# Kernel tuning notes

Measured on AMD Instinct MI355X. Metric: run time of the kernel, lower is better.

Reference implementation:

```python
import jax, jax.numpy as jnp
import numpy as np

jax.config.update("jax_enable_x64", True)  # hash arithmetic needs 64-bit ints

P = 56598313          # RzLinear.P (prime for the hash)
INPUT_DIM = 4096
OUTPUT_DIM = 4096
COMPRESS_RATIO = 0.0625
HASH_SIZE = int(INPUT_DIM * OUTPUT_DIM * COMPRESS_RATIO)  # 1,048,576
N_TOKENS = 8192


def setup_inputs() -> dict:
    key = jax.random.key(0)
    kx, kw, kr = jax.random.split(key, 3)
    x = jax.random.normal(kx, (N_TOKENS, INPUT_DIM), dtype=jnp.float32)
    hashed_weight = jax.random.normal(kw, (HASH_SIZE,), dtype=jnp.float32) * 0.02
    # _generate_random_numbers: [P, r1, r2, r3] with r_i forced even via r + r % 2
    r = jax.random.randint(kr, (3,), 0, P, dtype=jnp.int64)
    r = r + r % 2
    random_numbers = jnp.concatenate([jnp.array([P], dtype=jnp.int64), r])
    bias = jnp.zeros((OUTPUT_DIM,), dtype=jnp.float32)
    return {"x": x, "hashed_weight": hashed_weight,
            "random_numbers": random_numbers, "bias": bias}


def _hash_indices(random_numbers):
    # ROBE-Z hash (chunk_size=1): idx[k, n] = ((k*r3 + n*r2 + r1) % P) % HASH_SIZE
    r0 = random_numbers[0]
    r1 = random_numbers[1]
    r2 = random_numbers[2]
    r3 = random_numbers[3]
    k = jnp.arange(INPUT_DIM, dtype=jnp.int64)[:, None]   # (K, 1)
    n = jnp.arange(OUTPUT_DIM, dtype=jnp.int64)[None, :]  # (1, N)
    return ((k * r3 + n * r2 + r1) % r0) % HASH_SIZE       # (K, N)


def reference(x, hashed_weight, random_numbers, bias):
    idx = _hash_indices(random_numbers)
    W = hashed_weight[idx]          # gather-reconstructed (input_dim, output_dim)
    return x @ W + bias             # (N_TOKENS, output_dim)
```

## Files before the change

### kernel.cpp

```cpp
#include <hip/hip_runtime.h>
#include <stdint.h>


#define P_CONST 56598313u
#define HASH_MASK 0xFFFFFu
#define M_DIM 8192
#define N_DIM 4096
#define K_DIM 4096
#define BK 32
#define KSTEPS (K_DIM / BK)

typedef __attribute__((ext_vector_type(8))) short bf16x8;
typedef __attribute__((ext_vector_type(4))) float f32x4;
typedef __attribute__((ext_vector_type(4))) unsigned int u32x4;

__device__ __forceinline__ unsigned short f2bf(float f) {
    unsigned int u = __float_as_uint(f);
    return (unsigned short)((u + 0x7FFFu + ((u >> 16) & 1u)) >> 16);
}

struct RN { unsigned long long r1, r2, r3; };

__device__ __forceinline__ RN decode_rn(const void* rn_raw) {
    RN o;
    const long long* rn64 = (const long long*)rn_raw;
    if (rn64[0] == 56598313LL) {
        o.r1 = (unsigned long long)rn64[1];
        o.r2 = (unsigned long long)rn64[2];
        o.r3 = (unsigned long long)rn64[3];
    } else {
        const int* rn32 = (const int*)rn_raw;
        o.r1 = (unsigned long long)(unsigned int)rn32[1];
        o.r2 = (unsigned long long)(unsigned int)rn32[2];
        o.r3 = (unsigned long long)(unsigned int)rn32[3];
    }
    return o;
}

__device__ __forceinline__ void load16(const void* g, void* l) {
    __builtin_amdgcn_global_load_lds(
        (const __attribute__((address_space(1))) void*)g,
        (__attribute__((address_space(3))) void*)l,
        16, 0, 0);
}

__global__ __launch_bounds__(256) void prep(const float* __restrict__ x,
                                            const float* __restrict__ table,
                                            const void* __restrict__ rn_raw,
                                            unsigned short* __restrict__ Wt,
                                            unsigned short* __restrict__ Xb) {
    const int b = blockIdx.x;
    const int t = threadIdx.x;
    if (b % 5 == 0) {
        RN rn = decode_rn(rn_raw);
        const unsigned int stepu = (unsigned int)(rn.r3 % P_CONST);
        const unsigned int n = (unsigned int)(b / 5);
        const unsigned long long base =
            ((unsigned long long)n * rn.r2 + rn.r1) % P_CONST;
        const int k0 = t * 8;
        unsigned int c0 =
            (unsigned int)((base + (unsigned long long)k0 * stepu) % P_CONST);
        unsigned int c1 =
            (unsigned int)((base + (unsigned long long)(k0 + 2048) * stepu) % P_CONST);
        float f[16];
#pragma unroll
        for (int i = 0; i < 8; ++i) {
            f[i] = table[c0 & HASH_MASK];
            c0 += stepu; if (c0 >= P_CONST) c0 -= P_CONST;
            f[8 + i] = table[c1 & HASH_MASK];
            c1 += stepu; if (c1 >= P_CONST) c1 -= P_CONST;
        }
        union { unsigned short s[8]; u32x4 v; } o0, o1;
#pragma unroll
        for (int i = 0; i < 8; ++i) { o0.s[i] = f2bf(f[i]); o1.s[i] = f2bf(f[8 + i]); }
        unsigned short* dst = Wt + (size_t)n * K_DIM + k0;
        __builtin_nontemporal_store(o0.v, (u32x4*)dst);
        __builtin_nontemporal_store(o1.v, (u32x4*)(dst + 2048));
    } else {
        const int cb = b - b / 5 - 1;
        const size_t i8 = ((size_t)cb * 256 + t) * 8;
        const f32x4 a = __builtin_nontemporal_load((const f32x4*)(x + i8));
        const f32x4 c = __builtin_nontemporal_load((const f32x4*)(x + i8 + 4));
        union { unsigned short s[8]; u32x4 v; } o;
        o.s[0] = f2bf(a.x); o.s[1] = f2bf(a.y); o.s[2] = f2bf(a.z); o.s[3] = f2bf(a.w);
        o.s[4] = f2bf(c.x); o.s[5] = f2bf(c.y); o.s[6] = f2bf(c.z); o.s[7] = f2bf(c.w);
        __builtin_nontemporal_store(o.v, (u32x4*)(Xb + i8));
    }
}

__global__ __launch_bounds__(512, 2) void gemm_bt8(
    const unsigned short* __restrict__ A,
    const unsigned short* __restrict__ Bt,
    const float* __restrict__ bias,
    float* __restrict__ C) {
    __shared__ __align__(16) unsigned short lA[4][256 * BK];
    __shared__ __align__(16) unsigned short lB[4][256 * BK];

    const int t = threadIdx.x;
    const int bid0 = blockIdx.x;
    const int sb = (bid0 & 7) * 64 + (bid0 >> 3);
    const int m0 = (sb >> 4) * 256;
    const int n0 = (sb & 15) * 256;

    const int lane = t & 63;
    const int wid = t >> 6;
    const int wr = wid >> 2;
    const int wc = wid & 3;
    const int lm = lane & 15;
    const int q = lane >> 4;
    const int qswz = (q ^ ((lm >> 1) & 3)) << 4;

    const int p0 = t * 16;
    const int p1 = p0 + 8192;
    const int l0 = p0 ^ ((p0 >> 3) & 0x30);
    const int l1 = p1 ^ ((p1 >> 3) & 0x30);
    const int r0 = l0 >> 6, c0 = (l0 & 63) >> 1;
    const int r1 = l1 >> 6, c1 = (l1 & 63) >> 1;

    const unsigned short* Abase = A + (size_t)m0 * K_DIM;
    const unsigned short* Bbase = Bt + (size_t)n0 * K_DIM;

    f32x4 acc[8][4] = {};

#define STAGE_A(KS) do { const int b__ = (KS) & 3;                              \
    load16(Abase + (size_t)r0 * K_DIM + (KS) * BK + c0, (char*)&lA[b__][0] + p0);\
    load16(Abase + (size_t)r1 * K_DIM + (KS) * BK + c1, (char*)&lA[b__][0] + p1);\
} while (0)
#define STAGE_B(KS) do { const int b__ = (KS) & 3;                              \
    load16(Bbase + (size_t)r0 * K_DIM + (KS) * BK + c0, (char*)&lB[b__][0] + p0);\
    load16(Bbase + (size_t)r1 * K_DIM + (KS) * BK + c1, (char*)&lB[b__][0] + p1);\
} while (0)

#define STEP_BODY(KS, STG) do {                                                 \
    __builtin_amdgcn_s_barrier();                                               \
    asm volatile("" ::: "memory");                                              \
    const char* bufA = (const char*)&lA[(KS) & 3][0];                           \
    const char* bufB = (const char*)&lB[(KS) & 3][0];                           \
    bf16x8 af[8], bfr[4];                                                       \
    _Pragma("unroll")                                                           \
    for (int i = 0; i < 8; ++i)                                                 \
        af[i] = *(const bf16x8*)(bufA + (((wr * 128 + i * 16 + lm) << 6) | qswz));\
    _Pragma("unroll")                                                           \
    for (int j = 0; j < 4; ++j)                                                 \
        bfr[j] = *(const bf16x8*)(bufB + (((wc * 64 + j * 16 + lm) << 6) | qswz));\
    if (STG) { STAGE_A((KS) + 3); STAGE_B((KS) + 3); }                          \
    asm volatile("s_waitcnt lgkmcnt(0)" ::: "memory");                          \
    __builtin_amdgcn_sched_barrier(0);                                          \
    __builtin_amdgcn_s_setprio(1);                                              \
    _Pragma("unroll")                                                           \
    for (int i = 0; i < 8; ++i)                                                 \
        _Pragma("unroll")                                                       \
        for (int j = 0; j < 4; ++j)                                             \
            acc[i][j] = __builtin_amdgcn_mfma_f32_16x16x32_bf16(                \
                af[i], bfr[j], acc[i][j], 0, 0, 0);                             \
    __builtin_amdgcn_s_setprio(0);                                              \
} while (0)

    STAGE_A(0); STAGE_B(0);
    STAGE_A(1); STAGE_B(1);
    STAGE_A(2); STAGE_B(2);

#pragma unroll 1
    for (int ks = 0; ks < KSTEPS - 2; ++ks) {
        asm volatile("s_waitcnt vmcnt(8)" ::: "memory");
        STEP_BODY(ks, (ks < KSTEPS - 3));
    }
    asm volatile("s_waitcnt vmcnt(4)" ::: "memory");
    STEP_BODY(KSTEPS - 2, false);
    asm volatile("s_waitcnt vmcnt(0)" ::: "memory");
    STEP_BODY(KSTEPS - 1, false);

#undef STEP_BODY
#undef STAGE_A
#undef STAGE_B

#pragma unroll
    for (int j = 0; j < 4; ++j) {
        const int col = n0 + wc * 64 + j * 16 + lm;
        const float bv = bias[col];
#pragma unroll
        for (int i = 0; i < 8; ++i) {
            const int row = m0 + wr * 128 + i * 16 + q * 4;
#pragma unroll
            for (int r = 0; r < 4; ++r)
                __builtin_nontemporal_store(
                    acc[i][j][r] + bv, &C[(size_t)(row + r) * N_DIM + col]);
        }
    }
}

__global__ __launch_bounds__(256) void gemm_fused(const float* __restrict__ X,
                                                  const float* __restrict__ table,
                                                  const void* __restrict__ rn_raw,
                                                  const float* __restrict__ bias,
                                                  float* __restrict__ C) {
    RN rn = decode_rn(rn_raw);
    const unsigned int stepu = (unsigned int)(rn.r3 % P_CONST);
    const unsigned int step32 =
        (unsigned int)(((unsigned long long)stepu * 32ull) % P_CONST);

    __shared__ __align__(16) unsigned short lA[128 * 32];
    __shared__ __align__(16) unsigned short lB[128 * 32];
    const int t = threadIdx.x;
    const int m0 = blockIdx.y * 128;
    const int n0 = blockIdx.x * 128;
    const int lane = t & 63;
    const int w = t >> 6;
    const int wr = w >> 1, wc = w & 1;
    const int lm = lane & 15, q = lane >> 4;

    unsigned int curB[2];
    int rowB[2], colB[2];
#pragma unroll
    for (int e = 0; e < 2; ++e) {
        const int c = t + e * 256;
        rowB[e] = c >> 2;
        colB[e] = (c & 3) * 8;
        const unsigned long long base =
            ((unsigned long long)(n0 + rowB[e]) * rn.r2 + rn.r1) % P_CONST;
        curB[e] =
            (unsigned int)((base + (unsigned long long)colB[e] * stepu) % P_CONST);
    }

    f32x4 acc[4][4] = {};

    for (int k0 = 0; k0 < K_DIM; k0 += 32) {
#pragma unroll
        for (int c = t; c < 1024; c += 256) {
            const int row = c >> 3, col = (c & 7) * 4;
            const float4 v =
                *(const float4*)(X + (size_t)(m0 + row) * K_DIM + k0 + col);
            ushort4 o;
            o.x = f2bf(v.x); o.y = f2bf(v.y); o.z = f2bf(v.z); o.w = f2bf(v.w);
            *(ushort4*)&lA[row * 32 + col] = o;
        }
#pragma unroll
        for (int e = 0; e < 2; ++e) {
            unsigned int cur = curB[e];
            union { unsigned short s[8]; uint4 v; } o;
#pragma unroll
            for (int i = 0; i < 8; ++i) {
                o.s[i] = f2bf(table[cur & HASH_MASK]);
                cur += stepu;
                if (cur >= P_CONST) cur -= P_CONST;
            }
            curB[e] += step32;
            if (curB[e] >= P_CONST) curB[e] -= P_CONST;
            *(uint4*)&lB[rowB[e] * 32 + colB[e]] = o.v;
        }
        __syncthreads();

        bf16x8 af[4], bfr[4];
#pragma unroll
        for (int i = 0; i < 4; ++i)
            af[i] = *(const bf16x8*)&lA[(wr * 64 + i * 16 + lm) * 32 + q * 8];
#pragma unroll
        for (int j = 0; j < 4; ++j)
            bfr[j] = *(const bf16x8*)&lB[(wc * 64 + j * 16 + lm) * 32 + q * 8];
#pragma unroll
        for (int i = 0; i < 4; ++i)
#pragma unroll
            for (int j = 0; j < 4; ++j)
                acc[i][j] = __builtin_amdgcn_mfma_f32_16x16x32_bf16(
                    af[i], bfr[j], acc[i][j], 0, 0, 0);
        __syncthreads();
    }

#pragma unroll
    for (int j = 0; j < 4; ++j) {
        const int col = n0 + wc * 64 + j * 16 + lm;
        const float bv = bias[col];
#pragma unroll
        for (int i = 0; i < 4; ++i) {
            const int row = m0 + wr * 64 + i * 16 + q * 4;
#pragma unroll
            for (int r = 0; r < 4; ++r)
                C[(size_t)(row + r) * N_DIM + col] = acc[i][j][r] + bv;
        }
    }
}

extern "C" void kernel_launch(void* const* d_in, const int* in_sizes, int n_in,
                              void* d_out, int out_size, void* d_ws, size_t ws_size,
                              hipStream_t stream) {
    const float* x = (const float*)d_in[0];
    const float* hw = (const float*)d_in[1];
    const void* rn = d_in[2];
    const float* bias = (const float*)d_in[3];
    float* out = (float*)d_out;

    const size_t wt_bytes = (size_t)N_DIM * K_DIM * 2;
    const size_t xb_bytes = (size_t)M_DIM * K_DIM * 2;

    if (ws_size >= wt_bytes + xb_bytes) {
        unsigned short* Wt = (unsigned short*)d_ws;
        unsigned short* Xb = (unsigned short*)((char*)d_ws + wt_bytes);
        prep<<<20480, 256, 0, stream>>>(x, hw, rn, Wt, Xb);
        gemm_bt8<<<dim3((M_DIM / 256) * (N_DIM / 256)), 512, 0, stream>>>(Xb, Wt, bias, out);
    } else {
        gemm_fused<<<dim3(N_DIM / 128, M_DIM / 128), 256, 0, stream>>>(x, hw, rn, bias, out);
    }
}
```

Baseline: 556.3 us.

## Restructure GEMM pipeline to 64-wide K tiles and merge prep block roles

The GEMM main loop moves from a 4-deep ring of 32-wide K slices to double-buffered 64-wide K tiles, each split into two halves. Compute is interleaved in quarter-tile MFMA groups with more barriers, and the next tile is issued in two stages. The prep kernel stops splitting blocks between weight gathering and x conversion; every block now does both, gathering 4 weight entries and converting 8 x values per thread. The aim is fewer loop iterations and balanced prep work, at the cost of a shallower prefetch distance and extra barriers per tile.

New measurement: 636.7 us. 1.14x slower.

```diff
diff --git a/kernel.cpp b/kernel.cpp
--- a/kernel.cpp
+++ b/kernel.cpp
@@ -7,12 +7,12 @@
 #define M_DIM 8192
 #define N_DIM 4096
 #define K_DIM 4096
-#define BK 32
-#define KSTEPS (K_DIM / BK)
+#define KT (K_DIM / 64)
 
 typedef __attribute__((ext_vector_type(8))) short bf16x8;
 typedef __attribute__((ext_vector_type(4))) float f32x4;
 typedef __attribute__((ext_vector_type(4))) unsigned int u32x4;
+typedef __attribute__((ext_vector_type(2))) unsigned int u32x2;
 
 __device__ __forceinline__ unsigned short f2bf(float f) {
     unsigned int u = __float_as_uint(f);
@@ -51,50 +51,40 @@
                                             unsigned short* __restrict__ Xb) {
     const int b = blockIdx.x;
     const int t = threadIdx.x;
-    if (b % 5 == 0) {
-        RN rn = decode_rn(rn_raw);
-        const unsigned int stepu = (unsigned int)(rn.r3 % P_CONST);
-        const unsigned int n = (unsigned int)(b / 5);
-        const unsigned long long base =
-            ((unsigned long long)n * rn.r2 + rn.r1) % P_CONST;
-        const int k0 = t * 8;
-        unsigned int c0 =
-            (unsigned int)((base + (unsigned long long)k0 * stepu) % P_CONST);
-        unsigned int c1 =
-            (unsigned int)((base + (unsigned long long)(k0 + 2048) * stepu) % P_CONST);
-        float f[16];
-#pragma unroll
-        for (int i = 0; i < 8; ++i) {
-            f[i] = table[c0 & HASH_MASK];
-            c0 += stepu; if (c0 >= P_CONST) c0 -= P_CONST;
-            f[8 + i] = table[c1 & HASH_MASK];
-            c1 += stepu; if (c1 >= P_CONST) c1 -= P_CONST;
-        }
-        union { unsigned short s[8]; u32x4 v; } o0, o1;
-#pragma unroll
-        for (int i = 0; i < 8; ++i) { o0.s[i] = f2bf(f[i]); o1.s[i] = f2bf(f[8 + i]); }
-        unsigned short* dst = Wt + (size_t)n * K_DIM + k0;
-        __builtin_nontemporal_store(o0.v, (u32x4*)dst);
-        __builtin_nontemporal_store(o1.v, (u32x4*)(dst + 2048));
-    } else {
-        const int cb = b - b / 5 - 1;
-        const size_t i8 = ((size_t)cb * 256 + t) * 8;
-        const f32x4 a = __builtin_nontemporal_load((const f32x4*)(x + i8));
-        const f32x4 c = __builtin_nontemporal_load((const f32x4*)(x + i8 + 4));
-        union { unsigned short s[8]; u32x4 v; } o;
-        o.s[0] = f2bf(a.x); o.s[1] = f2bf(a.y); o.s[2] = f2bf(a.z); o.s[3] = f2bf(a.w);
-        o.s[4] = f2bf(c.x); o.s[5] = f2bf(c.y); o.s[6] = f2bf(c.z); o.s[7] = f2bf(c.w);
-        __builtin_nontemporal_store(o.v, (u32x4*)(Xb + i8));
-    }
-}
-
-__global__ __launch_bounds__(512, 2) void gemm_bt8(
+    RN rn = decode_rn(rn_raw);
+    const unsigned int stepu = (unsigned int)(rn.r3 % P_CONST);
+    const unsigned int n = (unsigned int)(b >> 2);
+    const int kb = ((b & 3) << 10) + (t << 2);
+    const unsigned long long base =
+        ((unsigned long long)n * rn.r2 + rn.r1) % P_CONST;
+    unsigned int cur =
+        (unsigned int)((base + (unsigned long long)kb * stepu) % P_CONST);
+    const float g0 = table[cur & HASH_MASK];
+    cur += stepu; if (cur >= P_CONST) cur -= P_CONST;
+    const float g1 = table[cur & HASH_MASK];
+    cur += stepu; if (cur >= P_CONST) cur -= P_CONST;
+    const float g2 = table[cur & HASH_MASK];
+    cur += stepu; if (cur >= P_CONST) cur -= P_CONST;
+    const float g3 = table[cur & HASH_MASK];
+    const size_t i8 = ((size_t)b * 256 + t) * 8;
+    const f32x4 a = __builtin_nontemporal_load((const f32x4*)(x + i8));
+    const f32x4 c = __builtin_nontemporal_load((const f32x4*)(x + i8 + 4));
+    union { unsigned short s[8]; u32x4 v; } o;
+    o.s[0] = f2bf(a.x); o.s[1] = f2bf(a.y); o.s[2] = f2bf(a.z); o.s[3] = f2bf(a.w);
+    o.s[4] = f2bf(c.x); o.s[5] = f2bf(c.y); o.s[6] = f2bf(c.z); o.s[7] = f2bf(c.w);
+    __builtin_nontemporal_store(o.v, (u32x4*)(Xb + i8));
+    union { unsigned short s[4]; u32x2 v; } w;
+    w.s[0] = f2bf(g0); w.s[1] = f2bf(g1); w.s[2] = f2bf(g2); w.s[3] = f2bf(g3);
+    __builtin_nontemporal_store(w.v, (u32x2*)(Wt + (size_t)n * K_DIM + kb));
+}
+
+__global__ __launch_bounds__(512, 2) void gemm_bt64(
     const unsigned short* __restrict__ A,
     const unsigned short* __restrict__ Bt,
     const float* __restrict__ bias,
     float* __restrict__ C) {
-    __shared__ __align__(16) unsigned short lA[4][256 * BK];
-    __shared__ __align__(16) unsigned short lB[4][256 * BK];
+    __shared__ __align__(16) unsigned short lA[2][2][256 * 32];
+    __shared__ __align__(16) unsigned short lB[2][2][256 * 32];
 
     const int t = threadIdx.x;
     const int bid0 = blockIdx.x;
@@ -122,57 +112,96 @@
 
     f32x4 acc[8][4] = {};
 
-#define STAGE_A(KS) do { const int b__ = (KS) & 3;                              \
-    load16(Abase + (size_t)r0 * K_DIM + (KS) * BK + c0, (char*)&lA[b__][0] + p0);\
-    load16(Abase + (size_t)r1 * K_DIM + (KS) * BK + c1, (char*)&lA[b__][0] + p1);\
+#define STAGE(T, KH) do {                                                       \
+    const int db__ = (T) & 1;                                                   \
+    const size_t ko__ = (size_t)(T) * 64 + (KH) * 32;                           \
+    load16(Abase + (size_t)r0 * K_DIM + ko__ + c0, (char*)&lA[db__][KH][0] + p0);\
+    load16(Abase + (size_t)r1 * K_DIM + ko__ + c1, (char*)&lA[db__][KH][0] + p1);\
+    load16(Bbase + (size_t)r0 * K_DIM + ko__ + c0, (char*)&lB[db__][KH][0] + p0);\
+    load16(Bbase + (size_t)r1 * K_DIM + ko__ + c1, (char*)&lB[db__][KH][0] + p1);\
 } while (0)
-#define STAGE_B(KS) do { const int b__ = (KS) & 3;                              \
-    load16(Bbase + (size_t)r0 * K_DIM + (KS) * BK + c0, (char*)&lB[b__][0] + p0);\
-    load16(Bbase + (size_t)r1 * K_DIM + (KS) * BK + c1, (char*)&lB[b__][0] + p1);\
+
+#define MFMA16(JB) do {                                                         \
+    _Pragma("unroll")                                                           \
+    for (int i = 0; i < 8; ++i) {                                               \
+        acc[i][JB] = __builtin_amdgcn_mfma_f32_16x16x32_bf16(                   \
+            af[i], bq0, acc[i][JB], 0, 0, 0);                                   \
+        acc[i][(JB) + 1] = __builtin_amdgcn_mfma_f32_16x16x32_bf16(             \
+            af[i], bq1, acc[i][(JB) + 1], 0, 0, 0);                             \
+    }                                                                           \
 } while (0)
 
-#define STEP_BODY(KS, STG) do {                                                 \
-    __builtin_amdgcn_s_barrier();                                               \
-    asm volatile("" ::: "memory");                                              \
-    const char* bufA = (const char*)&lA[(KS) & 3][0];                           \
-    const char* bufB = (const char*)&lB[(KS) & 3][0];                           \
-    bf16x8 af[8], bfr[4];                                                       \
-    _Pragma("unroll")                                                           \
-    for (int i = 0; i < 8; ++i)                                                 \
-        af[i] = *(const bf16x8*)(bufA + (((wr * 128 + i * 16 + lm) << 6) | qswz));\
-    _Pragma("unroll")                                                           \
-    for (int j = 0; j < 4; ++j)                                                 \
-        bfr[j] = *(const bf16x8*)(bufB + (((wc * 64 + j * 16 + lm) << 6) | qswz));\
-    if (STG) { STAGE_A((KS) + 3); STAGE_B((KS) + 3); }                          \
-    asm volatile("s_waitcnt lgkmcnt(0)" ::: "memory");                          \
-    __builtin_amdgcn_sched_barrier(0);                                          \
-    __builtin_amdgcn_s_setprio(1);                                              \
-    _Pragma("unroll")                                                           \
-    for (int i = 0; i < 8; ++i)                                                 \
-        _Pragma("unroll")                                                       \
-        for (int j = 0; j < 4; ++j)                                             \
-            acc[i][j] = __builtin_amdgcn_mfma_f32_16x16x32_bf16(                \
-                af[i], bfr[j], acc[i][j], 0, 0, 0);                             \
-    __builtin_amdgcn_s_setprio(0);                                              \
-} while (0)
-
-    STAGE_A(0); STAGE_B(0);
-    STAGE_A(1); STAGE_B(1);
-    STAGE_A(2); STAGE_B(2);
+#define BAR() do { __builtin_amdgcn_s_barrier();                                \
+                   asm volatile("" ::: "memory"); } while (0)
+#define LGKM0() do { asm volatile("s_waitcnt lgkmcnt(0)" ::: "memory");         \
+                     __builtin_amdgcn_sched_barrier(0); } while (0)
+
+    STAGE(0, 0);
+    STAGE(0, 1);
+    asm volatile("s_waitcnt vmcnt(4)" ::: "memory");
+    BAR();
 
 #pragma unroll 1
-    for (int ks = 0; ks < KSTEPS - 2; ++ks) {
-        asm volatile("s_waitcnt vmcnt(8)" ::: "memory");
-        STEP_BODY(ks, (ks < KSTEPS - 3));
-    }
-    asm volatile("s_waitcnt vmcnt(4)" ::: "memory");
-    STEP_BODY(KSTEPS - 2, false);
-    asm volatile("s_waitcnt vmcnt(0)" ::: "memory");
-    STEP_BODY(KSTEPS - 1, false);
-
-#undef STEP_BODY
-#undef STAGE_A
-#undef STAGE_B
+    for (int tt = 0; tt < KT; ++tt) {
+        const int db = tt & 1;
+        const char* a0 = (const char*)&lA[db][0][0];
+        const char* a1 = (const char*)&lA[db][1][0];
+        const char* b0 = (const char*)&lB[db][0][0];
+        const char* b1 = (const char*)&lB[db][1][0];
+        bf16x8 af[8], bq0, bq1;
+
+#pragma unroll
+        for (int i = 0; i < 8; ++i)
+            af[i] = *(const bf16x8*)(a0 + (((wr * 128 + i * 16 + lm) << 6) | qswz));
+        bq0 = *(const bf16x8*)(b0 + (((wc * 64 + 0 * 16 + lm) << 6) | qswz));
+        bq1 = *(const bf16x8*)(b0 + (((wc * 64 + 1 * 16 + lm) << 6) | qswz));
+        if (tt + 1 < KT) STAGE(tt + 1, 0);
+        BAR();
+        LGKM0();
+        __builtin_amdgcn_s_setprio(1);
+        MFMA16(0);
+        __builtin_amdgcn_s_setprio(0);
+        BAR();
+
+        bq0 = *(const bf16x8*)(b0 + (((wc * 64 + 2 * 16 + lm) << 6) | qswz));
+        bq1 = *(const bf16x8*)(b0 + (((wc * 64 + 3 * 16 + lm) << 6) | qswz));
+        if (tt + 1 < KT) STAGE(tt + 1, 1);
+        BAR();
+        LGKM0();
+        __builtin_amdgcn_s_setprio(1);
+        MFMA16(2);
+        __builtin_amdgcn_s_setprio(0);
+        if (tt == KT - 1) asm volatile("s_waitcnt vmcnt(0)" ::: "memory");
+        else              asm volatile("s_waitcnt vmcnt(8)" ::: "memory");
+        BAR();
+
+#pragma unroll
+        for (int i = 0; i < 8; ++i)
+            af[i] = *(const bf16x8*)(a1 + (((wr * 128 + i * 16 + lm) << 6) | qswz));
+        bq0 = *(const bf16x8*)(b1 + (((wc * 64 + 0 * 16 + lm) << 6) | qswz));
+        bq1 = *(const bf16x8*)(b1 + (((wc * 64 + 1 * 16 + lm) << 6) | qswz));
+        BAR();
+        LGKM0();
+        __builtin_amdgcn_s_setprio(1);
+        MFMA16(0);
+        __builtin_amdgcn_s_setprio(0);
+        BAR();
+
+        bq0 = *(const bf16x8*)(b1 + (((wc * 64 + 2 * 16 + lm) << 6) | qswz));
+        bq1 = *(const bf16x8*)(b1 + (((wc * 64 + 3 * 16 + lm) << 6) | qswz));
+        BAR();
+        LGKM0();
+        __builtin_amdgcn_s_setprio(1);
+        MFMA16(2);
+        __builtin_amdgcn_s_setprio(0);
+        asm volatile("s_waitcnt vmcnt(4)" ::: "memory");
+        BAR();
+    }
+
+#undef STAGE
+#undef MFMA16
+#undef BAR
+#undef LGKM0
 
 #pragma unroll
     for (int j = 0; j < 4; ++j) {
@@ -295,8 +324,8 @@
     if (ws_size >= wt_bytes + xb_bytes) {
         unsigned short* Wt = (unsigned short*)d_ws;
         unsigned short* Xb = (unsigned short*)((char*)d_ws + wt_bytes);
-        prep<<<20480, 256, 0, stream>>>(x, hw, rn, Wt, Xb);
-        gemm_bt8<<<dim3((M_DIM / 256) * (N_DIM / 256)), 512, 0, stream>>>(Xb, Wt, bias, out);
+        prep<<<16384, 256, 0, stream>>>(x, hw, rn, Wt, Xb);
+        gemm_bt64<<<dim3((M_DIM / 256) * (N_DIM / 256)), 512, 0, stream>>>(Xb, Wt, bias, out);
     } else {
         gemm_fused<<<dim3(N_DIM / 128, M_DIM / 128), 256, 0, stream>>>(x, hw, rn, bias, out);
     }
```
